# Kernel optimization log

Measured on AMD Instinct MI355X. Metric: run time of the kernel, lower is better.

The kernel has to match this reference:

```python
import jax, jax.numpy as jnp
import numpy as np

N, E = 50000, 800000
DN, DE, H = 128, 64, 8
C = DN // H  # per-head dim = 16


def setup_inputs() -> dict:
    key = jax.random.key(0)
    ks = jax.random.split(key, 16)
    s = 0.05
    inp = {
        "node_state": jax.random.normal(ks[0], (N, DN), jnp.float32),
        "edge_index": jax.random.randint(ks[1], (2, E), 0, N, jnp.int64 if jax.config.jax_enable_x64 else jnp.int32),
        "edge_state": jax.random.normal(ks[2], (E, DE), jnp.float32),
        # edge_proj: Linear(DE, DE)
        "W_edge": jax.random.normal(ks[3], (DE, DE), jnp.float32) * s,
        "b_edge": jnp.zeros((DE,), jnp.float32),
        # TransformerConv linears (in, out) layout: y = x @ W + b
        "Wq": jax.random.normal(ks[4], (DN, DN), jnp.float32) * s,
        "bq": jnp.zeros((DN,), jnp.float32),
        "Wk": jax.random.normal(ks[5], (DN, DN), jnp.float32) * s,
        "bk": jnp.zeros((DN,), jnp.float32),
        "Wv": jax.random.normal(ks[6], (DN, DN), jnp.float32) * s,
        "bv": jnp.zeros((DN,), jnp.float32),
        "We": jax.random.normal(ks[7], (DE, DN), jnp.float32) * s,  # lin_edge, no bias
        "Wskip": jax.random.normal(ks[8], (DN, DN), jnp.float32) * s,
        "bskip": jnp.zeros((DN,), jnp.float32),
        "Wbeta": jax.random.normal(ks[9], (3 * DN, 1), jnp.float32) * s,  # lin_beta, no bias
        "ln_g": jnp.ones((DN,), jnp.float32),
        "ln_b": jnp.zeros((DN,), jnp.float32),
    }
    return inp


def reference(node_state, edge_index, edge_state, W_edge, b_edge, Wq, bq, Wk, bk,
              Wv, bv, We, Wskip, bskip, Wbeta, ln_g, ln_b):
    n = node_state.shape[0]
    src, dst = edge_index[0], edge_index[1]

    # edge_proj
    edge_attr = edge_state @ W_edge + b_edge  # [E, DE]

    # TransformerConv (beta=True, concat=True, dropout in eval mode)
    q = (node_state @ Wq + bq).reshape(n, H, C)
    k = (node_state @ Wk + bk).reshape(n, H, C)
    v = (node_state @ Wv + bv).reshape(n, H, C)
    e = (edge_attr @ We).reshape(-1, H, C)  # [E, H, C]

    kj = k[src] + e                                        # [E, H, C]
    alpha = jnp.sum(q[dst] * kj, axis=-1) / np.sqrt(C)     # [E, H]

    # segment softmax over destination nodes
    amax = jax.ops.segment_max(alpha, dst, num_segments=n)  # [N, H]
    ex = jnp.exp(alpha - amax[dst])
    denom = jax.ops.segment_sum(ex, dst, num_segments=n)    # [N, H]
    a = ex / denom[dst]                                     # [E, H]

    msg = (v[src] + e) * a[:, :, None]                      # [E, H, C]
    out = jax.ops.segment_sum(msg, dst, num_segments=n).reshape(n, DN)

    # beta-gated skip
    x_r = node_state @ Wskip + bskip
    beta = jax.nn.sigmoid(jnp.concatenate([out, x_r, out - x_r], axis=-1) @ Wbeta)  # [N, 1]
    out = beta * x_r + (1.0 - beta) * out

    # LayerNorm
    mu = jnp.mean(out, axis=-1, keepdims=True)
    var = jnp.mean(jnp.square(out - mu), axis=-1, keepdims=True)
    normed = (out - mu) * jax.lax.rsqrt(var + 1e-5) * ln_g + ln_b

    # residual + relu (dropout is identity in eval)
    return node_state + jax.nn.relu(normed)
```

## Files before the change

### kernel.cpp

```cpp
#include <hip/hip_runtime.h>
#include <cstdint>
#include <cstddef>

#define NN 50000
#define NE 800000

#define NNT ((NN + 63)/64)
#define NET (NE/64)

typedef short bf16x8 __attribute__((ext_vector_type(8)));
typedef float f32x4 __attribute__((ext_vector_type(4)));
typedef float f32x2 __attribute__((ext_vector_type(2)));

__device__ __forceinline__ float b2f(unsigned short s) {
  union { unsigned int u; float f; } x; x.u = ((unsigned int)s) << 16; return x.f;
}
__device__ __forceinline__ unsigned short f2b(float f) {
  union { float f; unsigned int u; } x; x.f = f;
  unsigned int r = x.u + 0x7FFFu + ((x.u >> 16) & 1u);
  return (unsigned short)(r >> 16);
}

#define WS_WCE    0u
#define WS_BCE    16384u
#define WS_WCEF   20480u
#define WS_WALLF  40960u
#define WS_BALL   172032u
#define WS_QB     180224u
#define WS_KB     12980224u
#define WS_VB     25780224u
#define WS_XR     38580224u
#define WS_EB     64180224u
#define WS_CNT    268980224u
#define WS_OFF    269180224u
#define WS_CUR    269380224u
#define WS_BSUM   269580224u
#define WS_POS    269584320u
#define WS_SRCS   272784320u

__global__ void k_prep(const float* __restrict__ W_edge, const float* __restrict__ b_edge,
                       const float* __restrict__ We, unsigned short* __restrict__ wce,
                       float* __restrict__ bce) {
  int i = blockIdx.x;
  int j = threadIdx.x;
  float s = 0.f;
  for (int m = 0; m < 64; ++m) s += W_edge[i*64+m] * We[m*128+j];
  wce[i*128+j] = f2b(s);
  if (i == 0) {
    float bb = 0.f;
    for (int m = 0; m < 64; ++m) bb += b_edge[m] * We[m*128+j];
    bce[j] = bb;
  }
}

__global__ void k_pack_wce(const unsigned short* __restrict__ wce, unsigned short* __restrict__ wcef) {
  int fb = blockIdx.x;
  int ct = fb >> 1, s = fb & 1;
  int l = threadIdx.x;
  unsigned short* dst = wcef + (((size_t)(ct*2+s))*64 + l)*8;
  int col = ct*16 + (l & 15);
  int k0 = s*32 + (l >> 4)*8;
  #pragma unroll
  for (int j = 0; j < 8; ++j) dst[j] = wce[(k0+j)*128 + col];
}

__global__ void k_pack_wall(const float* __restrict__ Wq, const float* __restrict__ Wk,
                            const float* __restrict__ Wv, const float* __restrict__ Ws,
                            unsigned short* __restrict__ wallf) {
  int fb = blockIdx.x;
  int mat = fb >> 5, ct = (fb >> 2) & 7, s = fb & 3;
  int l = threadIdx.x;
  const float* W = (mat==0) ? Wq : (mat==1) ? Wk : (mat==2) ? Wv : Ws;
  unsigned short* dst = wallf + ((((size_t)(mat*8+ct))*4 + s)*64 + l)*8;
  int col = ct*16 + (l & 15);
  int k0 = s*32 + (l >> 4)*8;
  #pragma unroll
  for (int j = 0; j < 8; ++j) dst[j] = f2b(W[(k0+j)*128 + col]);
}

__global__ void k_pack_bias(const float* __restrict__ bq, const float* __restrict__ bk,
                            const float* __restrict__ bv, const float* __restrict__ bs,
                            float* __restrict__ ball) {
  int m = blockIdx.x, c = threadIdx.x;
  const float* b = (m==0) ? bq : (m==1) ? bk : (m==2) ? bv : bs;
  ball[m*128 + c] = b[c];
}

__global__ void __launch_bounds__(256) k_mfma_all(
    const float* __restrict__ x, const unsigned short* __restrict__ wallf,
    const float* __restrict__ ball,
    unsigned short* __restrict__ qb, unsigned char* __restrict__ kb,
    unsigned char* __restrict__ vb, float* __restrict__ xr,
    const float* __restrict__ es, const unsigned short* __restrict__ wcef,
    const float* __restrict__ bce, const int* __restrict__ pos,
    unsigned char* __restrict__ eb) {
  __shared__ char smem[18688];
  int b = blockIdx.x;
  int l = threadIdx.x & 63, w = threadIdx.x >> 6;
  int g = l >> 4, ln = l & 15;

  if (b % 17 == 0) {
    int tile = b / 17;
    if (tile >= NNT) return;
    int n0 = tile * 64;
    unsigned short* sA = (unsigned short*)smem;
    for (int i = 0; i < 4; ++i) {
      int c = threadIdx.x + i*256;
      int row = c >> 4, ch = c & 15;
      int sw = (ch & 8) | ((ch & 7) ^ (row & 7));
      unsigned short tmp[8];
      if (n0 + row < NN) {
        const float* src = x + (size_t)(n0+row)*128 + ch*8;
        float4 f0 = *(const float4*)src;
        float4 f1 = *(const float4*)(src + 4);
        tmp[0]=f2b(f0.x); tmp[1]=f2b(f0.y); tmp[2]=f2b(f0.z); tmp[3]=f2b(f0.w);
        tmp[4]=f2b(f1.x); tmp[5]=f2b(f1.y); tmp[6]=f2b(f1.z); tmp[7]=f2b(f1.w);
      } else {
        #pragma unroll
        for (int j = 0; j < 8; ++j) tmp[j] = 0;
      }
      *(uint4*)&sA[row*128 + sw*8] = *(const uint4*)tmp;
    }
    __syncthreads();
    int row = w*16 + ln;
    int node = n0 + row;
    bf16x8 bfr[4];
    #pragma unroll
    for (int s = 0; s < 4; ++s) {
      int ch = s*4 + g;
      int sw = (ch & 8) | ((ch & 7) ^ (row & 7));
      bfr[s] = *(const bf16x8*)&sA[row*128 + sw*8];
    }
    for (int mat = 0; mat < 4; ++mat) {
      f32x4 acc[8];
      #pragma unroll
      for (int ct = 0; ct < 8; ++ct) acc[ct] = (f32x4){0.f,0.f,0.f,0.f};
      #pragma unroll
      for (int s = 0; s < 4; ++s) {
        #pragma unroll
        for (int ct = 0; ct < 8; ++ct) {
          bf16x8 wf = *(const bf16x8*)(wallf + ((((size_t)(mat*8+ct))*4 + s)*64 + l)*8);
          acc[ct] = __builtin_amdgcn_mfma_f32_16x16x32_bf16(wf, bfr[s], acc[ct], 0, 0, 0);
        }
      }
      if (node < NN) {
        #pragma unroll
        for (int ct = 0; ct < 8; ++ct) {
          int c0 = ct*16 + g*4;
          float4 bi = *(const float4*)(ball + mat*128 + c0);
          float v0 = acc[ct][0] + bi.x, v1 = acc[ct][1] + bi.y;
          float v2 = acc[ct][2] + bi.z, v3 = acc[ct][3] + bi.w;
          if (mat == 3) {
            float4 o = {v0, v1, v2, v3};
            *(float4*)(xr + (size_t)node*128 + c0) = o;
          } else if (mat == 0) {
            unsigned short o[4] = {f2b(v0), f2b(v1), f2b(v2), f2b(v3)};
            *(uint2*)(qb + (size_t)node*128 + c0) = *(const uint2*)o;
          } else {
            int pk = 0;
            pk = __builtin_amdgcn_cvt_pk_fp8_f32(v0, v1, pk, false);
            pk = __builtin_amdgcn_cvt_pk_fp8_f32(v2, v3, pk, true);
            unsigned char* dst = (mat==1) ? kb : vb;
            *(int*)(dst + (size_t)node*128 + c0) = pk;
          }
        }
      }
    }
  } else {
    int tile = b - b/17 - 1;
    if (tile >= NET) return;
    int e0 = tile * 64;
    unsigned short* sA  = (unsigned short*)smem;
    unsigned char*  sO8 = (unsigned char*)(smem + 8192);
    int*            sP  = (int*)(smem + 18432);
    if (threadIdx.x < 64) sP[threadIdx.x] = pos[e0 + threadIdx.x];
    for (int i = 0; i < 2; ++i) {
      int c = threadIdx.x + i*256;
      int row = c >> 3, ch = c & 7;
      int sw = ch ^ (row & 7);
      const float* src = es + (size_t)(e0+row)*64 + ch*8;
      float4 f0 = *(const float4*)src;
      float4 f1 = *(const float4*)(src + 4);
      unsigned short tmp[8];
      tmp[0]=f2b(f0.x); tmp[1]=f2b(f0.y); tmp[2]=f2b(f0.z); tmp[3]=f2b(f0.w);
      tmp[4]=f2b(f1.x); tmp[5]=f2b(f1.y); tmp[6]=f2b(f1.z); tmp[7]=f2b(f1.w);
      *(uint4*)&sA[row*64 + sw*8] = *(const uint4*)tmp;
    }
    __syncthreads();
    f32x4 acc[8];
    #pragma unroll
    for (int ct = 0; ct < 8; ++ct) acc[ct] = (f32x4){0.f,0.f,0.f,0.f};
    int row = w*16 + ln;
    #pragma unroll
    for (int s = 0; s < 2; ++s) {
      int ch = (s*4 + g) ^ (row & 7);
      bf16x8 bfr = *(const bf16x8*)&sA[row*64 + ch*8];
      #pragma unroll
      for (int ct = 0; ct < 8; ++ct) {
        bf16x8 wf = *(const bf16x8*)(wcef + (((size_t)(ct*2+s))*64 + l)*8);
        acc[ct] = __builtin_amdgcn_mfma_f32_16x16x32_bf16(wf, bfr, acc[ct], 0, 0, 0);
      }
    }
    #pragma unroll
    for (int ct = 0; ct < 8; ++ct) {
      int c0 = ct*16 + g*4;
      float4 bi = *(const float4*)(bce + c0);
      int pk = 0;
      pk = __builtin_amdgcn_cvt_pk_fp8_f32(acc[ct][0]+bi.x, acc[ct][1]+bi.y, pk, false);
      pk = __builtin_amdgcn_cvt_pk_fp8_f32(acc[ct][2]+bi.z, acc[ct][3]+bi.w, pk, true);
      int ch = ct ^ (row & 7);
      *(int*)&sO8[row*160 + ch*16 + g*4] = pk;
    }
    __syncthreads();
    int rrow = threadIdx.x >> 3;
    int rch  = threadIdx.x & 7;
    #pragma unroll
    for (int it = 0; it < 2; ++it) {
      int r = it*32 + rrow;
      int swc = rch ^ (r & 7);
      uint4 val = *(const uint4*)&sO8[r*160 + swc*16];
      int prow = sP[r];
      *(uint4*)(eb + (size_t)prow*128 + rch*16) = val;
    }
  }
}

__global__ void __launch_bounds__(256) k_hist(const int* __restrict__ ei, int* __restrict__ cnt) {
  int t = blockIdx.x * 256 + threadIdx.x;
  if (t < NE) atomicAdd(&cnt[ei[NE + t]], 1);
}

__global__ void __launch_bounds__(256) k_scanA(const int* __restrict__ cnt,
    int* __restrict__ off, int* __restrict__ bsum) {
  __shared__ int s[256];
  int i = blockIdx.x * 256 + threadIdx.x;
  int v = (i < NN) ? cnt[i] : 0;
  s[threadIdx.x] = v;
  __syncthreads();
  #pragma unroll
  for (int d = 1; d < 256; d <<= 1) {
    int t = (threadIdx.x >= d) ? s[threadIdx.x - d] : 0;
    __syncthreads();
    s[threadIdx.x] += t;
    __syncthreads();
  }
  if (i < NN) off[i] = s[threadIdx.x] - v;
  if (threadIdx.x == 255) bsum[blockIdx.x] = s[255];
}

__global__ void __launch_bounds__(256) k_scanB(int* __restrict__ bsum, int nb) {
  __shared__ int s[256];
  int v = (threadIdx.x < nb) ? bsum[threadIdx.x] : 0;
  s[threadIdx.x] = v;
  __syncthreads();
  #pragma unroll
  for (int d = 1; d < 256; d <<= 1) {
    int t = (threadIdx.x >= d) ? s[threadIdx.x - d] : 0;
    __syncthreads();
    s[threadIdx.x] += t;
    __syncthreads();
  }
  if (threadIdx.x < nb) bsum[threadIdx.x] = s[threadIdx.x] - v;
}

__global__ void __launch_bounds__(256) k_scanC(int* __restrict__ off,
    const int* __restrict__ bsum, int* __restrict__ cur) {
  int i = blockIdx.x * 256 + threadIdx.x;
  if (i < NN) {
    int o = off[i] + bsum[blockIdx.x];
    off[i] = o;
    cur[i] = o;
  }
}

__global__ void __launch_bounds__(256) k_scatter(const int* __restrict__ ei,
    int* __restrict__ cur, int* __restrict__ pos, int* __restrict__ srcs) {
  int t = blockIdx.x * 256 + threadIdx.x;
  if (t < NE) {
    int d = ei[NE + t];
    int p = atomicAdd(&cur[d], 1);
    pos[t] = p;
    srcs[p] = ei[t];
  }
}

__global__ void __launch_bounds__(256) k_attn(
    const int* __restrict__ off, const int* __restrict__ cnt,
    const int* __restrict__ srcs,
    const unsigned short* __restrict__ qb, const unsigned char* __restrict__ kb,
    const unsigned char* __restrict__ vb, const unsigned char* __restrict__ eb,
    const float* __restrict__ xr, const float* __restrict__ x,
    const float* __restrict__ Wb, const float* __restrict__ ln_g,
    const float* __restrict__ ln_b, float* __restrict__ out) {
  int wid = threadIdx.x >> 6, lane = threadIdx.x & 63;
  int n = blockIdx.x * 4 + wid;
  if (n >= NN) return;
  int c = lane * 2;

  unsigned int qu = *(const unsigned int*)(qb + (size_t)n*128 + c);
  float q0 = b2f((unsigned short)(qu & 0xffffu)), q1 = b2f((unsigned short)(qu >> 16));

  int start = off[n], m = cnt[n];
  const int* sp = srcs + start;
  const unsigned char* ep = eb + (size_t)start*128 + c;
  float acc0 = 0.f, acc1 = 0.f, den = 0.f;

  auto body = [&](unsigned int ku2, unsigned int eu2, unsigned int vu2) {
    f32x2 ef = __builtin_amdgcn_cvt_pk_f32_fp8((int)eu2, false);
    f32x2 kf = __builtin_amdgcn_cvt_pk_f32_fp8((int)ku2, false);
    f32x2 vf = __builtin_amdgcn_cvt_pk_f32_fp8((int)vu2, false);
    float p = q0*(kf[0] + ef[0]) + q1*(kf[1] + ef[1]);
    p += __shfl_xor(p, 1);
    p += __shfl_xor(p, 2);
    p += __shfl_xor(p, 4);
    float a = __expf(p * 0.25f);
    den  += a;
    acc0 += a * (vf[0] + ef[0]);
    acc1 += a * (vf[1] + ef[1]);
  };

  int i = 0;
  for (; i + 8 <= m; i += 8) {
    int sn[8]; unsigned int eu[8], ku[8], vu[8];
    #pragma unroll
    for (int j = 0; j < 8; ++j) sn[j] = sp[i+j];
    #pragma unroll
    for (int j = 0; j < 8; ++j) eu[j] = *(const unsigned short*)(ep + (size_t)(i+j)*128);
    #pragma unroll
    for (int j = 0; j < 8; ++j) {
      ku[j] = *(const unsigned short*)(kb + (size_t)sn[j]*128 + c);
      vu[j] = *(const unsigned short*)(vb + (size_t)sn[j]*128 + c);
    }
    #pragma unroll
    for (int j = 0; j < 8; ++j) body(ku[j], eu[j], vu[j]);
  }
  for (; i + 4 <= m; i += 4) {
    int sn[4]; unsigned int eu[4], ku[4], vu[4];
    #pragma unroll
    for (int j = 0; j < 4; ++j) sn[j] = sp[i+j];
    #pragma unroll
    for (int j = 0; j < 4; ++j) eu[j] = *(const unsigned short*)(ep + (size_t)(i+j)*128);
    #pragma unroll
    for (int j = 0; j < 4; ++j) {
      ku[j] = *(const unsigned short*)(kb + (size_t)sn[j]*128 + c);
      vu[j] = *(const unsigned short*)(vb + (size_t)sn[j]*128 + c);
    }
    #pragma unroll
    for (int j = 0; j < 4; ++j) body(ku[j], eu[j], vu[j]);
  }
  for (; i < m; ++i) {
    int sA = sp[i];
    unsigned int euA = *(const unsigned short*)(ep + (size_t)i*128);
    unsigned int kuA = *(const unsigned short*)(kb + (size_t)sA*128 + c);
    unsigned int vuA = *(const unsigned short*)(vb + (size_t)sA*128 + c);
    body(kuA, euA, vuA);
  }

  float inv = (m > 0) ? 1.f / den : 0.f;
  float o0 = acc0 * inv, o1 = acc1 * inv;

  float2 r = *(const float2*)(xr + (size_t)n*128 + c);
  float p = o0*Wb[c] + o1*Wb[c+1] + r.x*Wb[128+c] + r.y*Wb[128+c+1]
          + (o0-r.x)*Wb[256+c] + (o1-r.y)*Wb[256+c+1];
  #pragma unroll
  for (int offs = 32; offs > 0; offs >>= 1) p += __shfl_xor(p, offs);
  float beta = 1.f / (1.f + __expf(-p));
  float g0 = beta*r.x + (1.f-beta)*o0;
  float g1 = beta*r.y + (1.f-beta)*o1;
  float msum = g0 + g1;
  #pragma unroll
  for (int offs = 32; offs > 0; offs >>= 1) msum += __shfl_xor(msum, offs);
  msum *= (1.f/128.f);
  float d0 = g0 - msum, d1 = g1 - msum;
  float vv = d0*d0 + d1*d1;
  #pragma unroll
  for (int offs = 32; offs > 0; offs >>= 1) vv += __shfl_xor(vv, offs);
  vv *= (1.f/128.f);
  float rs = rsqrtf(vv + 1e-5f);
  float n0 = d0*rs*ln_g[c]   + ln_b[c];
  float n1 = d1*rs*ln_g[c+1] + ln_b[c+1];
  float2 xv = *(const float2*)(x + (size_t)n*128 + c);
  float2 res;
  res.x = xv.x + fmaxf(n0, 0.f);
  res.y = xv.y + fmaxf(n1, 0.f);
  *(float2*)(out + (size_t)n*128 + c) = res;
}

extern "C" void kernel_launch(void* const* d_in, const int* in_sizes, int n_in,
                              void* d_out, int out_size, void* d_ws, size_t ws_size,
                              hipStream_t stream) {
  const float* node   = (const float*)d_in[0];
  const int*   ei     = (const int*)  d_in[1];
  const float* es     = (const float*)d_in[2];
  const float* W_edge = (const float*)d_in[3];
  const float* b_edge = (const float*)d_in[4];
  const float* Wq     = (const float*)d_in[5];
  const float* bq     = (const float*)d_in[6];
  const float* Wk     = (const float*)d_in[7];
  const float* bk     = (const float*)d_in[8];
  const float* Wv     = (const float*)d_in[9];
  const float* bv     = (const float*)d_in[10];
  const float* We     = (const float*)d_in[11];
  const float* Wskip  = (const float*)d_in[12];
  const float* bskip  = (const float*)d_in[13];
  const float* Wbeta  = (const float*)d_in[14];
  const float* ln_g   = (const float*)d_in[15];
  const float* ln_b   = (const float*)d_in[16];

  char* ws = (char*)d_ws;
  unsigned short* wce   = (unsigned short*)(ws + WS_WCE);
  float*          bce   = (float*)(ws + WS_BCE);
  unsigned short* wcef  = (unsigned short*)(ws + WS_WCEF);
  unsigned short* wallf = (unsigned short*)(ws + WS_WALLF);
  float*          ball  = (float*)(ws + WS_BALL);
  unsigned short* qb  = (unsigned short*)(ws + WS_QB);
  unsigned char*  kb  = (unsigned char*)(ws + WS_KB);
  unsigned char*  vb  = (unsigned char*)(ws + WS_VB);
  float*          xr  = (float*)(ws + WS_XR);
  unsigned char*  eb  = (unsigned char*)(ws + WS_EB);
  int*            cnt = (int*)(ws + WS_CNT);
  int*            off = (int*)(ws + WS_OFF);
  int*            cur = (int*)(ws + WS_CUR);
  int*            bsm = (int*)(ws + WS_BSUM);
  int*            pos = (int*)(ws + WS_POS);
  int*            srcs= (int*)(ws + WS_SRCS);

  hipMemsetAsync(cnt, 0, (size_t)NN*4, stream);

  k_prep<<<64, 128, 0, stream>>>(W_edge, b_edge, We, wce, bce);
  k_pack_wce<<<16, 64, 0, stream>>>(wce, wcef);
  k_pack_wall<<<128, 64, 0, stream>>>(Wq, Wk, Wv, Wskip, wallf);
  k_pack_bias<<<4, 128, 0, stream>>>(bq, bk, bv, bskip, ball);

  const int nbScan = (NN + 255)/256;
  k_hist<<<(NE + 255)/256, 256, 0, stream>>>(ei, cnt);
  k_scanA<<<nbScan, 256, 0, stream>>>(cnt, off, bsm);
  k_scanB<<<1, 256, 0, stream>>>(bsm, nbScan);
  k_scanC<<<nbScan, 256, 0, stream>>>(off, bsm, cur);
  k_scatter<<<(NE + 255)/256, 256, 0, stream>>>(ei, cur, pos, srcs);

  const int grid = 17 * NNT;
  k_mfma_all<<<grid, 256, 0, stream>>>(node, wallf, ball, qb, kb, vb, xr,
                                       es, wcef, bce, pos, eb);

  k_attn<<<(NN + 3)/4, 256, 0, stream>>>(off, cnt, srcs, qb, kb, vb, eb,
                                         xr, node, Wbeta, ln_g, ln_b, (float*)d_out);
}
```

Before: 291.7 us.

## Fuse weight prep kernels and load edge tiles directly into LDS

The four small weight-preparation kernels are merged into one launch that also folds W_edge·We straight into the packed MFMA fragment layout, so three launches and the intermediate wce buffer go away. In the edge-projection path, fp32 edge_state rows are now copied global-to-LDS with global_load_lds (swizzled through the source address), and the bf16 conversion happens when fragments are read from LDS instead of before the store. LDS is reused for the fp8 output staging, which needs an extra barrier. The aim is to cut launch overhead and register/VGPR staging on the large edge load, at the cost of twice the LDS bytes per tile and a redundant 64-term dot product per packed weight element.

```diff
diff --git a/kernel.cpp b/kernel.cpp
--- a/kernel.cpp
+++ b/kernel.cpp
@@ -11,6 +11,9 @@
 typedef short bf16x8 __attribute__((ext_vector_type(8)));
 typedef float f32x4 __attribute__((ext_vector_type(4)));
 typedef float f32x2 __attribute__((ext_vector_type(2)));
+
+#define GLB __attribute__((address_space(1)))
+#define LDS __attribute__((address_space(3)))
 
 __device__ __forceinline__ float b2f(unsigned short s) {
   union { unsigned int u; float f; } x; x.u = ((unsigned int)s) << 16; return x.f;
@@ -38,52 +41,53 @@
 #define WS_POS    269584320u
 #define WS_SRCS   272784320u
 
-__global__ void k_prep(const float* __restrict__ W_edge, const float* __restrict__ b_edge,
-                       const float* __restrict__ We, unsigned short* __restrict__ wce,
-                       float* __restrict__ bce) {
-  int i = blockIdx.x;
-  int j = threadIdx.x;
-  float s = 0.f;
-  for (int m = 0; m < 64; ++m) s += W_edge[i*64+m] * We[m*128+j];
-  wce[i*128+j] = f2b(s);
-  if (i == 0) {
-    float bb = 0.f;
-    for (int m = 0; m < 64; ++m) bb += b_edge[m] * We[m*128+j];
-    bce[j] = bb;
-  }
-}
-
-__global__ void k_pack_wce(const unsigned short* __restrict__ wce, unsigned short* __restrict__ wcef) {
-  int fb = blockIdx.x;
-  int ct = fb >> 1, s = fb & 1;
-  int l = threadIdx.x;
-  unsigned short* dst = wcef + (((size_t)(ct*2+s))*64 + l)*8;
-  int col = ct*16 + (l & 15);
-  int k0 = s*32 + (l >> 4)*8;
-  #pragma unroll
-  for (int j = 0; j < 8; ++j) dst[j] = wce[(k0+j)*128 + col];
-}
-
-__global__ void k_pack_wall(const float* __restrict__ Wq, const float* __restrict__ Wk,
-                            const float* __restrict__ Wv, const float* __restrict__ Ws,
-                            unsigned short* __restrict__ wallf) {
-  int fb = blockIdx.x;
-  int mat = fb >> 5, ct = (fb >> 2) & 7, s = fb & 3;
-  int l = threadIdx.x;
-  const float* W = (mat==0) ? Wq : (mat==1) ? Wk : (mat==2) ? Wv : Ws;
-  unsigned short* dst = wallf + ((((size_t)(mat*8+ct))*4 + s)*64 + l)*8;
-  int col = ct*16 + (l & 15);
-  int k0 = s*32 + (l >> 4)*8;
-  #pragma unroll
-  for (int j = 0; j < 8; ++j) dst[j] = f2b(W[(k0+j)*128 + col]);
-}
-
-__global__ void k_pack_bias(const float* __restrict__ bq, const float* __restrict__ bk,
-                            const float* __restrict__ bv, const float* __restrict__ bs,
-                            float* __restrict__ ball) {
-  int m = blockIdx.x, c = threadIdx.x;
-  const float* b = (m==0) ? bq : (m==1) ? bk : (m==2) ? bv : bs;
-  ball[m*128 + c] = b[c];
+__global__ void __launch_bounds__(128) k_prep_all(
+    const float* __restrict__ W_edge, const float* __restrict__ b_edge,
+    const float* __restrict__ We,
+    const float* __restrict__ Wq, const float* __restrict__ Wk,
+    const float* __restrict__ Wv, const float* __restrict__ Ws,
+    const float* __restrict__ bq, const float* __restrict__ bk,
+    const float* __restrict__ bv, const float* __restrict__ bs,
+    unsigned short* __restrict__ wcef, float* __restrict__ bce,
+    unsigned short* __restrict__ wallf, float* __restrict__ ball) {
+  int b = blockIdx.x;
+  if (b < 16) {
+    int ct = b >> 1, s = b & 1;
+    int l = threadIdx.x;
+    if (l < 64) {
+      unsigned short* dst = wcef + (((size_t)(ct*2+s))*64 + l)*8;
+      int col = ct*16 + (l & 15);
+      int k0 = s*32 + (l >> 4)*8;
+      #pragma unroll
+      for (int j = 0; j < 8; ++j) {
+        int k = k0 + j;
+        float acc = 0.f;
+        for (int m = 0; m < 64; ++m) acc += W_edge[k*64+m] * We[m*128+col];
+        dst[j] = f2b(acc);
+      }
+    }
+  } else if (b < 144) {
+    int fb = b - 16;
+    int mat = fb >> 5, ct = (fb >> 2) & 7, s = fb & 3;
+    int l = threadIdx.x;
+    if (l < 64) {
+      const float* W = (mat==0) ? Wq : (mat==1) ? Wk : (mat==2) ? Wv : Ws;
+      unsigned short* dst = wallf + ((((size_t)(mat*8+ct))*4 + s)*64 + l)*8;
+      int col = ct*16 + (l & 15);
+      int k0 = s*32 + (l >> 4)*8;
+      #pragma unroll
+      for (int j = 0; j < 8; ++j) dst[j] = f2b(W[(k0+j)*128 + col]);
+    }
+  } else if (b < 148) {
+    int m = b - 144, c = threadIdx.x;
+    const float* bb = (m==0) ? bq : (m==1) ? bk : (m==2) ? bv : bs;
+    ball[m*128 + c] = bb[c];
+  } else {
+    int col = threadIdx.x;
+    float acc = 0.f;
+    for (int m = 0; m < 64; ++m) acc += b_edge[m] * We[m*128+col];
+    bce[col] = acc;
+  }
 }
 
 __global__ void __launch_bounds__(256) k_mfma_all(
@@ -94,7 +98,7 @@
     const float* __restrict__ es, const unsigned short* __restrict__ wcef,
     const float* __restrict__ bce, const int* __restrict__ pos,
     unsigned char* __restrict__ eb) {
-  __shared__ char smem[18688];
+  __shared__ char smem[16640];
   int b = blockIdx.x;
   int l = threadIdx.x & 63, w = threadIdx.x >> 6;
   int g = l >> 4, ln = l & 15;
@@ -170,21 +174,25 @@
     int tile = b - b/17 - 1;
     if (tile >= NET) return;
     int e0 = tile * 64;
-    unsigned short* sA  = (unsigned short*)smem;
-    unsigned char*  sO8 = (unsigned char*)(smem + 8192);
-    int*            sP  = (int*)(smem + 18432);
+    char* sA8 = smem;
+    unsigned char* sO8 = (unsigned char*)smem;
+    int* sP = (int*)(smem + 16384);
     if (threadIdx.x < 64) sP[threadIdx.x] = pos[e0 + threadIdx.x];
-    for (int i = 0; i < 2; ++i) {
-      int c = threadIdx.x + i*256;
-      int row = c >> 3, ch = c & 7;
-      int sw = ch ^ (row & 7);
-      const float* src = es + (size_t)(e0+row)*64 + ch*8;
-      float4 f0 = *(const float4*)src;
-      float4 f1 = *(const float4*)(src + 4);
-      unsigned short tmp[8];
-      tmp[0]=f2b(f0.x); tmp[1]=f2b(f0.y); tmp[2]=f2b(f0.z); tmp[3]=f2b(f0.w);
-      tmp[4]=f2b(f1.x); tmp[5]=f2b(f1.y); tmp[6]=f2b(f1.z); tmp[7]=f2b(f1.w);
-      *(uint4*)&sA[row*64 + sw*8] = *(const uint4*)tmp;
+    {
+      int tt = threadIdx.x;
+      int rloc = tt >> 4;
+      int half = tt & 1;
+      int p = (tt & 15) >> 1;
+      #pragma unroll
+      for (int i = 0; i < 4; ++i) {
+        int row = i*16 + rloc;
+        int srcChunk = p ^ (row & 7);
+        const float* gsrc = es + (size_t)(e0 + row)*64 + srcChunk*8 + half*4;
+        __builtin_amdgcn_global_load_lds(
+            (const GLB unsigned int*)gsrc,
+            (LDS unsigned int*)(sA8 + i*4096 + w*1024 + l*16),
+            16, 0, 0);
+      }
     }
     __syncthreads();
     f32x4 acc[8];
@@ -193,14 +201,20 @@
     int row = w*16 + ln;
     #pragma unroll
     for (int s = 0; s < 2; ++s) {
-      int ch = (s*4 + g) ^ (row & 7);
-      bf16x8 bfr = *(const bf16x8*)&sA[row*64 + ch*8];
+      int chsw = (s*4 + g) ^ (row & 7);
+      const float* fsrc = (const float*)(sA8 + (size_t)row*256 + chsw*32);
+      float4 fa = *(const float4*)fsrc;
+      float4 fb2 = *(const float4*)(fsrc + 4);
+      unsigned short t8[8] = {f2b(fa.x), f2b(fa.y), f2b(fa.z), f2b(fa.w),
+                              f2b(fb2.x), f2b(fb2.y), f2b(fb2.z), f2b(fb2.w)};
+      bf16x8 bfr = *(const bf16x8*)t8;
       #pragma unroll
       for (int ct = 0; ct < 8; ++ct) {
         bf16x8 wf = *(const bf16x8*)(wcef + (((size_t)(ct*2+s))*64 + l)*8);
         acc[ct] = __builtin_amdgcn_mfma_f32_16x16x32_bf16(wf, bfr, acc[ct], 0, 0, 0);
       }
     }
+    __syncthreads();
     #pragma unroll
     for (int ct = 0; ct < 8; ++ct) {
       int c0 = ct*16 + g*4;
@@ -408,7 +422,6 @@
   const float* ln_b   = (const float*)d_in[16];
 
   char* ws = (char*)d_ws;
-  unsigned short* wce   = (unsigned short*)(ws + WS_WCE);
   float*          bce   = (float*)(ws + WS_BCE);
   unsigned short* wcef  = (unsigned short*)(ws + WS_WCEF);
   unsigned short* wallf = (unsigned short*)(ws + WS_WALLF);
@@ -427,10 +440,8 @@
 
   hipMemsetAsync(cnt, 0, (size_t)NN*4, stream);
 
-  k_prep<<<64, 128, 0, stream>>>(W_edge, b_edge, We, wce, bce);
-  k_pack_wce<<<16, 64, 0, stream>>>(wce, wcef);
-  k_pack_wall<<<128, 64, 0, stream>>>(Wq, Wk, Wv, Wskip, wallf);
-  k_pack_bias<<<4, 128, 0, stream>>>(bq, bk, bv, bskip, ball);
+  k_prep_all<<<149, 128, 0, stream>>>(W_edge, b_edge, We, Wq, Wk, Wv, Wskip,
+                                      bq, bk, bv, bskip, wcef, bce, wallf, ball);
 
   const int nbScan = (NN + 255)/256;
   k_hist<<<(NE + 255)/256, 256, 0, stream>>>(ei, cnt);
```

Measured after the change: 292.1 us. Within noise of the previous version (+0.1%).
